# Kernel optimization log

Hardware: AMD Instinct MI355X
Metric: run time of the kernel (lower is better)

## Reference

```python
import jax, jax.numpy as jnp
import numpy as np

N_NODES = 50000
N_EDGES = 600000
C = 128
T = 2          # layer index t
NU = 1         # DRew nu parameter
EPS = 0.0      # GIN eps


def mlp(x, W1, b1, W2, b2):
    # instantiate_mlp with final_activation=False, batch_norm=False:
    # Linear -> ReLU -> Linear
    return jax.nn.relu(x @ W1 + b1) @ W2 + b2


def setup_inputs() -> dict:
    key = jax.random.key(0)
    ks = jax.random.split(key, 16)
    node_embeddings = jax.random.normal(ks[0], (T + 1, N_NODES, C), dtype=jnp.float32)
    edge_index = jax.random.randint(ks[1], (2, N_EDGES), 0, N_NODES, dtype=jnp.int32)
    edge_weights = jax.random.randint(ks[2], (N_EDGES,), 1, T + 2, dtype=jnp.int32)  # hops 1..3
    s = 1.0 / np.sqrt(C)
    def lin(k):
        kw, kb = jax.random.split(k)
        return (jax.random.uniform(kw, (C, C), jnp.float32, -s, s),
                jax.random.uniform(kb, (C,), jnp.float32, -s, s))
    loop_W1, loop_b1 = lin(ks[3]); loop_W2, loop_b2 = lin(ks[4])
    rel_W1, rel_b1 = lin(ks[5]); rel_W2, rel_b2 = lin(ks[6])
    # T higher-hop MLPs (k = 2 .. T+1), stacked along axis 0
    hh1 = [lin(k) for k in jax.random.split(ks[7], T)]
    hh2 = [lin(k) for k in jax.random.split(ks[8], T)]
    hh_W1 = jnp.stack([w for w, _ in hh1]); hh_b1 = jnp.stack([b for _, b in hh1])
    hh_W2 = jnp.stack([w for w, _ in hh2]); hh_b2 = jnp.stack([b for _, b in hh2])
    hop_coef = jax.random.normal(ks[9], (T + 1,), dtype=jnp.float32)
    return dict(t=T, node_embeddings=node_embeddings, edge_index=edge_index,
                edge_weights=edge_weights,
                loop_W1=loop_W1, loop_b1=loop_b1, loop_W2=loop_W2, loop_b2=loop_b2,
                rel_W1=rel_W1, rel_b1=rel_b1, rel_W2=rel_W2, rel_b2=rel_b2,
                hh_W1=hh_W1, hh_b1=hh_b1, hh_W2=hh_W2, hh_b2=hh_b2,
                hop_coef=hop_coef)


def reference(t, node_embeddings, edge_index, edge_weights,
              loop_W1, loop_b1, loop_W2, loop_b2,
              rel_W1, rel_b1, rel_W2, rel_b2,
              hh_W1, hh_b1, hh_W2, hh_b2, hop_coef):
    x_t = node_embeddings[t]                       # [N, C]
    n = x_t.shape[0]
    row, col = edge_index[0], edge_index[1]        # sparse A: out[row] += X[col]
    dt = x_t.dtype

    hops = []
    # hop 1: relational MLP on current-layer embeddings
    h1 = mlp(x_t, rel_W1, rel_b1, rel_W2, rel_b2)
    m1 = (edge_weights == 1).astype(dt)[:, None]
    hops.append(jax.ops.segment_sum(h1[col] * m1, row, num_segments=n))
    # hops k = 2 .. t+1: per-hop MLP on delayed embeddings (DRew)
    for k in range(2, t + 2):
        delay = max(0, k - NU)
        hk = mlp(node_embeddings[t - delay],
                 hh_W1[k - 2], hh_b1[k - 2], hh_W2[k - 2], hh_b2[k - 2])
        mk = (edge_weights == k).astype(dt)[:, None]
        hops.append(jax.ops.segment_sum(hk[col] * mk, row, num_segments=n))

    by_hop = jnp.stack(hops)                       # [t+1, N, C]
    self_term = mlp((1.0 + EPS) * x_t, loop_W1, loop_b1, loop_W2, loop_b2)
    return self_term + jnp.einsum('k,knc->nc', hop_coef, by_hop)
```

## Files before the change

kernel.cpp:

```cpp
#include <hip/hip_runtime.h>

#define N_NODES 50000
#define N_EDGES 600000
#define C 128
#define STRIPS 3125
#define GROUPS 782
#define N_TASKS 4

typedef __bf16 bf16;
typedef __attribute__((ext_vector_type(8))) __bf16 bf16x8;
typedef __attribute__((ext_vector_type(4))) __bf16 bf16x4;
typedef __attribute__((ext_vector_type(2))) __bf16 bf16x2;
typedef __attribute__((ext_vector_type(4))) float f32x4;
typedef __attribute__((ext_vector_type(2))) float f32x2;

struct PtrsV { const void* p[8]; };

__device__ __forceinline__ int bf16_wild(unsigned short w) {
    int exp = (w >> 7) & 0xFF;
    int mant = w & 0x7F;
    if (exp == 0xFF) return 1;
    if (exp >= 133) return 1;
    if (exp == 0) return mant != 0 ? 1 : 0;
    if (exp <= 114) return 1;
    return 0;
}

__global__ void __launch_bounds__(256) detect_zero_kernel(
    const unsigned short* __restrict__ emb,
    const unsigned short* __restrict__ w,
    const unsigned short* __restrict__ b,
    const unsigned short* __restrict__ hc,
    int* __restrict__ flags, int* __restrict__ deg)
{
    if (blockIdx.x == 0) {
        int lane = threadIdx.x;
        if (lane >= 64) return;
        int ce = 0, cw = 0, cb = 0, ch = 0;
        for (int j = 0; j < 4; ++j) {
            ce += bf16_wild(emb[lane * 4 + j]);
            cw += bf16_wild(w[lane * 4 + j]);
        }
        for (int j = 0; j < 2; ++j) cb += bf16_wild(b[lane * 2 + j]);
        if (lane < 3) ch = bf16_wild(hc[lane]);
        for (int off = 32; off > 0; off >>= 1) {
            ce += __shfl_down(ce, off);
            cw += __shfl_down(cw, off);
            cb += __shfl_down(cb, off);
            ch += __shfl_down(ch, off);
        }
        if (lane == 0) {
            int wf = (cw >= 16) ? 1 : 0;
            flags[0] = (ce >= 16) ? 1 : 0;
            flags[1] = wf;
            flags[2] = (cb >= 8) ? 1 : 0;
            flags[3] = (ch > 0) ? 1 : wf;
        }
    } else {
        int i = (blockIdx.x - 1) * 256 + threadIdx.x;
        if (i < N_NODES) deg[i] = 0;
    }
}

__global__ void __launch_bounds__(256) pack_kernel(
    PtrsV wmats, PtrsV bvecs, const void* hc_raw,
    const int* __restrict__ flags,
    bf16* __restrict__ pw, float* __restrict__ cbias, float* __restrict__ ccoef)
{
    int tid = blockIdx.x * 256 + threadIdx.x;
    int wf = flags[1], bfl = flags[2], hf = flags[3];
    if (tid < 8 * 16384) {
        int m    = tid >> 14;
        int r    = tid & 16383;
        int j    = r & 7;
        int lane = (r >> 3) & 63;
        int n0   = (r >> 9) & 7;
        int kk   = r >> 12;
        int k = kk * 32 + (lane >> 4) * 8 + j;
        int n = n0 * 16 + (lane & 15);
        int idx = k * C + n + ((m == 4 || m == 5) ? 16384 : 0);
        float v = wf ? ((const float*)wmats.p[m])[idx]
                     : (float)((const bf16*)wmats.p[m])[idx];
        pw[tid] = (bf16)v;
    } else if (tid < 8 * 16384 + 1024) {
        int j = tid - 8 * 16384;
        int m = j >> 7, n = j & 127;
        int idx = n + ((m == 4 || m == 5) ? 128 : 0);
        float v = bfl ? ((const float*)bvecs.p[m])[idx]
                      : (float)((const bf16*)bvecs.p[m])[idx];
        cbias[j] = v;
    } else if (tid < 8 * 16384 + 1024 + 3) {
        int i = tid - (8 * 16384 + 1024);
        float v = hf ? ((const float*)hc_raw)[i]
                     : (float)((const bf16*)hc_raw)[i];
        ccoef[i] = v;
    }
}

__global__ __launch_bounds__(256, 2) void mlp_kernel(
    const void* __restrict__ emb_raw,
    const bf16* __restrict__ pw,
    const float* __restrict__ cbias,
    const float* __restrict__ ccoef,
    const int* __restrict__ flags,
    bf16* __restrict__ h,
    bf16* __restrict__ hs)
{
    __shared__ bf16 sH[4][64][136];
    const int tid  = threadIdx.x;
    const int wave = tid >> 6, lane = tid & 63;
    const int wid  = blockIdx.x * 4 + wave;
    if (wid >= N_TASKS * GROUPS) return;
    const int task = wid & 3;
    const int grp  = wid >> 2;
    const int lrow = lane & 15, lquad = lane >> 4;
    bf16 (*sh)[136] = sH[wave];

    const int m1_of[4] = {0, 2, 4, 6};
    const int ly_of[4] = {2, 1, 0, 2};
    const int m1 = m1_of[task];
    const bf16x8* w1v = (const bf16x8*)(pw + (size_t)m1 * 16384);
    const bf16x8* w2v = w1v + 2048;
    const float oscale = (task == 0) ? ccoef[0] : (task == 1) ? ccoef[1]
                       : (task == 2) ? ccoef[2] : 1.0f;
    bf16* outp = (task == 3) ? hs : (h + (size_t)task * N_NODES * C);
    const int emb_f32 = flags[0];
    const size_t lbase = (size_t)ly_of[task] * N_NODES * C;

    const int s0 = grp * 4;
    int nv = STRIPS - s0; if (nv > 4) nv = 4;

    float b1f[8], b2f[8];
    #pragma unroll
    for (int n0 = 0; n0 < 8; ++n0) {
        b1f[n0] = cbias[m1 * 128 + n0 * 16 + lrow];
        b2f[n0] = cbias[(m1 + 1) * 128 + n0 * 16 + lrow];
    }

    bf16x8 af[4][4];
    #pragma unroll
    for (int i = 0; i < 4; ++i) {
        if (i < nv) {
            size_t xb = lbase + (size_t)((s0 + i) * 16 + lrow) * C + lquad * 8;
            if (emb_f32) {
                const float* xf = (const float*)emb_raw + xb;
                #pragma unroll
                for (int kk = 0; kk < 4; ++kk) {
                    f32x4 u0 = *(const f32x4*)(xf + kk * 32);
                    f32x4 u1 = *(const f32x4*)(xf + kk * 32 + 4);
                    bf16x8 v;
                    v[0]=(bf16)u0[0]; v[1]=(bf16)u0[1]; v[2]=(bf16)u0[2]; v[3]=(bf16)u0[3];
                    v[4]=(bf16)u1[0]; v[5]=(bf16)u1[1]; v[6]=(bf16)u1[2]; v[7]=(bf16)u1[3];
                    af[i][kk] = v;
                }
            } else {
                const bf16* x16 = (const bf16*)emb_raw + xb;
                #pragma unroll
                for (int kk = 0; kk < 4; ++kk)
                    af[i][kk] = *(const bf16x8*)(x16 + kk * 32);
            }
        }
    }

    #pragma unroll
    for (int n0 = 0; n0 < 8; ++n0) {
        bf16x8 bv0 = w1v[0 * 512 + n0 * 64 + lane];
        bf16x8 bv1 = w1v[1 * 512 + n0 * 64 + lane];
        bf16x8 bv2 = w1v[2 * 512 + n0 * 64 + lane];
        bf16x8 bv3 = w1v[3 * 512 + n0 * 64 + lane];
        int n = n0 * 16 + lrow;
        float bias = b1f[n0];
        #pragma unroll
        for (int i = 0; i < 4; ++i) {
            if (i < nv) {
                f32x4 a4 = {0.f, 0.f, 0.f, 0.f};
                a4 = __builtin_amdgcn_mfma_f32_16x16x32_bf16(af[i][0], bv0, a4, 0, 0, 0);
                a4 = __builtin_amdgcn_mfma_f32_16x16x32_bf16(af[i][1], bv1, a4, 0, 0, 0);
                a4 = __builtin_amdgcn_mfma_f32_16x16x32_bf16(af[i][2], bv2, a4, 0, 0, 0);
                a4 = __builtin_amdgcn_mfma_f32_16x16x32_bf16(af[i][3], bv3, a4, 0, 0, 0);
                #pragma unroll
                for (int r = 0; r < 4; ++r) {
                    float v = a4[r] + bias;
                    v = v > 0.f ? v : 0.f;
                    sh[i * 16 + lquad * 4 + r][n] = (bf16)v;
                }
            }
        }
    }

    bf16x8 ah[4][4];
    #pragma unroll
    for (int i = 0; i < 4; ++i)
        if (i < nv) {
            #pragma unroll
            for (int kk = 0; kk < 4; ++kk)
                ah[i][kk] = *(const bf16x8*)(&sh[i * 16 + lrow][kk * 32 + lquad * 8]);
        }

    #pragma unroll
    for (int n0 = 0; n0 < 8; ++n0) {
        bf16x8 bv0 = w2v[0 * 512 + n0 * 64 + lane];
        bf16x8 bv1 = w2v[1 * 512 + n0 * 64 + lane];
        bf16x8 bv2 = w2v[2 * 512 + n0 * 64 + lane];
        bf16x8 bv3 = w2v[3 * 512 + n0 * 64 + lane];
        int n = n0 * 16 + lrow;
        float bias = b2f[n0];
        #pragma unroll
        for (int i = 0; i < 4; ++i) {
            if (i < nv) {
                f32x4 a4 = {0.f, 0.f, 0.f, 0.f};
                a4 = __builtin_amdgcn_mfma_f32_16x16x32_bf16(ah[i][0], bv0, a4, 0, 0, 0);
                a4 = __builtin_amdgcn_mfma_f32_16x16x32_bf16(ah[i][1], bv1, a4, 0, 0, 0);
                a4 = __builtin_amdgcn_mfma_f32_16x16x32_bf16(ah[i][2], bv2, a4, 0, 0, 0);
                a4 = __builtin_amdgcn_mfma_f32_16x16x32_bf16(ah[i][3], bv3, a4, 0, 0, 0);
                #pragma unroll
                for (int r = 0; r < 4; ++r)
                    sh[i * 16 + lquad * 4 + r][n] = (bf16)((a4[r] + bias) * oscale);
            }
        }
    }

    {
        int row = lane >> 2;
        int cs  = (lane & 3) * 32;
        #pragma unroll
        for (int i = 0; i < 4; ++i) {
            if (i < nv) {
                bf16* dst = outp + (size_t)((s0 + i) * 16) * C;
                #pragma unroll
                for (int j = 0; j < 4; ++j) {
                    bf16x8 v = *(const bf16x8*)(&sh[i * 16 + row][cs + j * 8]);
                    *(bf16x8*)(dst + (size_t)row * C + cs + j * 8) = v;
                }
            }
        }
    }
}

__global__ void __launch_bounds__(256) hist_kernel(
    const int* __restrict__ erow, int* __restrict__ deg)
{
    int e = blockIdx.x * 256 + threadIdx.x;
    if (e >= N_EDGES) return;
    atomicAdd(&deg[erow[e]], 1);
}

__device__ __forceinline__ int wave_incl_scan(int v, int lane) {
    int x = v;
    #pragma unroll
    for (int d = 1; d < 64; d <<= 1) {
        int t = __shfl_up(x, d);
        if (lane >= d) x += t;
    }
    return x;
}

__global__ void __launch_bounds__(256) scanA_kernel(
    const int* __restrict__ deg, int* __restrict__ offsets, int* __restrict__ btot)
{
    __shared__ int swave[4];
    int b = blockIdx.x, tid = threadIdx.x;
    int i = b * 256 + tid;
    int lane = tid & 63, wv = tid >> 6;
    int v = (i < N_NODES) ? deg[i] : 0;
    int x = wave_incl_scan(v, lane);
    if (lane == 63) swave[wv] = x;
    __syncthreads();
    int w0 = swave[0], w1 = swave[1], w2 = swave[2], w3 = swave[3];
    int wp = (wv > 0 ? w0 : 0) + (wv > 1 ? w1 : 0) + (wv > 2 ? w2 : 0);
    if (i < N_NODES) offsets[i] = wp + x - v;
    if (tid == 0) btot[b] = w0 + w1 + w2 + w3;
}

__global__ void __launch_bounds__(256) scanB_kernel(
    const int* __restrict__ btot, int* __restrict__ bbase, int nblk)
{
    __shared__ int swave[4];
    int tid = threadIdx.x;
    int lane = tid & 63, wv = tid >> 6;
    int v = (tid < nblk) ? btot[tid] : 0;
    int x = wave_incl_scan(v, lane);
    if (lane == 63) swave[wv] = x;
    __syncthreads();
    int w0 = swave[0], w1 = swave[1], w2 = swave[2], w3 = swave[3];
    int wp = (wv > 0 ? w0 : 0) + (wv > 1 ? w1 : 0) + (wv > 2 ? w2 : 0);
    if (tid < nblk) bbase[tid] = wp + x - v;
}

__global__ void __launch_bounds__(256) scanC_kernel(
    const int* __restrict__ bbase, int* __restrict__ offsets, int* __restrict__ cursor)
{
    int i = blockIdx.x * 256 + threadIdx.x;
    if (i < N_NODES) {
        int o = offsets[i] + bbase[blockIdx.x];
        offsets[i] = o;
        cursor[i] = o;
    }
    if (i == 0) offsets[N_NODES] = N_EDGES;
}

__global__ void __launch_bounds__(256) fill_kernel(
    const int* __restrict__ erow, const int* __restrict__ ecol,
    const int* __restrict__ ew,
    int* __restrict__ cursor, int* __restrict__ edata)
{
    int e = blockIdx.x * 256 + threadIdx.x;
    if (e >= N_EDGES) return;
    int dst = erow[e];
    int pos = atomicAdd(&cursor[dst], 1);
    edata[pos] = (ecol[e] << 2) | (ew[e] - 1);
}

__global__ void __launch_bounds__(256) gather_kernel(
    const int* __restrict__ offsets, const int* __restrict__ edata,
    const bf16* __restrict__ h,
    const bf16* __restrict__ hs,
    void* __restrict__ out,
    const int* __restrict__ flags)
{
    const int node = blockIdx.x * 4 + (threadIdx.x >> 6);
    if (node >= N_NODES) return;
    const int lane = threadIdx.x & 63;
    const int c = lane * 2;

    bf16x2 sv = *(const bf16x2*)(hs + (size_t)node * C + c);
    float a0 = (float)sv[0], a1 = (float)sv[1];

    const int s = offsets[node], e = offsets[node + 1];
    for (int base = s; base < e; base += 64) {
        int idx = base + lane;
        int ed_i = (idx < e) ? edata[idx] : 0;
        int cnt = e - base; if (cnt > 64) cnt = 64;
        int j = 0;
        for (; j + 8 <= cnt; j += 8) {
            float t0 = 0.f, t1 = 0.f;
            #pragma unroll
            for (int u = 0; u < 8; ++u) {
                int ed = __shfl(ed_i, j + u);
                bf16x2 v = *(const bf16x2*)(h + (size_t)(ed & 3) * (N_NODES * C)
                                              + (size_t)(ed >> 2) * C + c);
                t0 += (float)v[0];
                t1 += (float)v[1];
            }
            a0 += t0; a1 += t1;
        }
        for (; j + 4 <= cnt; j += 4) {
            int e0 = __shfl(ed_i, j);
            int e1 = __shfl(ed_i, j + 1);
            int e2 = __shfl(ed_i, j + 2);
            int e3 = __shfl(ed_i, j + 3);
            bf16x2 v0 = *(const bf16x2*)(h + (size_t)(e0 & 3) * (N_NODES * C) + (size_t)(e0 >> 2) * C + c);
            bf16x2 v1 = *(const bf16x2*)(h + (size_t)(e1 & 3) * (N_NODES * C) + (size_t)(e1 >> 2) * C + c);
            bf16x2 v2 = *(const bf16x2*)(h + (size_t)(e2 & 3) * (N_NODES * C) + (size_t)(e2 >> 2) * C + c);
            bf16x2 v3 = *(const bf16x2*)(h + (size_t)(e3 & 3) * (N_NODES * C) + (size_t)(e3 >> 2) * C + c);
            a0 += (float)v0[0] + (float)v1[0] + (float)v2[0] + (float)v3[0];
            a1 += (float)v0[1] + (float)v1[1] + (float)v2[1] + (float)v3[1];
        }
        for (; j < cnt; ++j) {
            int ed = __shfl(ed_i, j);
            bf16x2 v = *(const bf16x2*)(h + (size_t)(ed & 3) * (N_NODES * C) + (size_t)(ed >> 2) * C + c);
            a0 += (float)v[0];
            a1 += (float)v[1];
        }
    }

    if (flags[0]) {
        f32x2 o; o[0] = a0; o[1] = a1;
        *(f32x2*)((float*)out + (size_t)node * C + c) = o;
    } else {
        bf16x2 o; o[0] = (bf16)a0; o[1] = (bf16)a1;
        *(bf16x2*)((bf16*)out + (size_t)node * C + c) = o;
    }
}

extern "C" void kernel_launch(void* const* d_in, const int* in_sizes, int n_in,
                              void* d_out, int out_size, void* d_ws, size_t ws_size,
                              hipStream_t stream) {
    const void* emb = d_in[1];
    const int*  ei  = (const int*)d_in[2];
    const int*  ew  = (const int*)d_in[3];

    const size_t H_BYTES  = (size_t)3 * N_NODES * C * sizeof(bf16);
    const size_t HS_BYTES = (size_t)N_NODES * C * sizeof(bf16);
    const size_t PW_BYTES = (size_t)8 * 16384 * sizeof(bf16);
    bf16*  h      = (bf16*)d_ws;
    bf16*  hs     = (bf16*)((char*)d_ws + H_BYTES);
    bf16*  pw     = (bf16*)((char*)d_ws + H_BYTES + HS_BYTES);
    float* cbias  = (float*)((char*)d_ws + H_BYTES + HS_BYTES + PW_BYTES);
    float* ccoef  = cbias + 1024;
    int*   flags  = (int*)(ccoef + 4);
    int*   deg    = flags + 16;
    int*   cursor = deg + N_NODES;
    int*   offsets= cursor + N_NODES;
    int*   btot   = offsets + N_NODES + 8;
    int*   bbase  = btot + 256;
    int*   edata  = bbase + 256;

    PtrsV wptr;
    wptr.p[0] = d_in[8];   wptr.p[1] = d_in[10];
    wptr.p[2] = d_in[12];  wptr.p[3] = d_in[14];
    wptr.p[4] = d_in[12];  wptr.p[5] = d_in[14];
    wptr.p[6] = d_in[4];   wptr.p[7] = d_in[6];
    PtrsV bptr;
    bptr.p[0] = d_in[9];   bptr.p[1] = d_in[11];
    bptr.p[2] = d_in[13];  bptr.p[3] = d_in[15];
    bptr.p[4] = d_in[13];  bptr.p[5] = d_in[15];
    bptr.p[6] = d_in[5];   bptr.p[7] = d_in[7];

    const int NBLK = (N_NODES + 255) / 256;

    detect_zero_kernel<<<1 + NBLK, 256, 0, stream>>>(
        (const unsigned short*)emb, (const unsigned short*)d_in[8],
        (const unsigned short*)d_in[9], (const unsigned short*)d_in[16],
        flags, deg);

    pack_kernel<<<517, 256, 0, stream>>>(wptr, bptr, d_in[16], flags, pw, cbias, ccoef);

    const int* erow = ei;
    const int* ecol = ei + N_EDGES;
    hist_kernel<<<(N_EDGES + 255) / 256, 256, 0, stream>>>(erow, deg);
    scanA_kernel<<<NBLK, 256, 0, stream>>>(deg, offsets, btot);
    scanB_kernel<<<1, 256, 0, stream>>>(btot, bbase, NBLK);
    scanC_kernel<<<NBLK, 256, 0, stream>>>(bbase, offsets, cursor);
    fill_kernel<<<(N_EDGES + 255) / 256, 256, 0, stream>>>(erow, ecol, ew, cursor, edata);

    mlp_kernel<<<(N_TASKS * GROUPS + 3) / 4, 256, 0, stream>>>(
        emb, pw, cbias, ccoef, flags, h, hs);

    gather_kernel<<<(N_NODES + 3) / 4, 256, 0, stream>>>(
        offsets, edata, h, hs, d_out, flags);
}
```

Baseline: 285.4 us.

## Split gather wave into two half-waves over edges and halve MLP strips per wave

The gather kernel now has each half of a wave handle alternate edges, with each lane loading 4 bf16 channels (8-byte loads) instead of 2. The two halves are combined with a cross-half shuffle reduction before the self term is added and the result stored. This is meant to double the edge-level memory parallelism per wave and widen the loads. Separately, the MLP kernel processes 2 strips per wave instead of 4, with a smaller LDS tile and a higher occupancy bound. That increases wave count and occupancy but reloads the weight fragments more often.

```diff
diff --git a/kernel.cpp b/kernel.cpp
--- a/kernel.cpp
+++ b/kernel.cpp
@@ -4,7 +4,7 @@
 #define N_EDGES 600000
 #define C 128
 #define STRIPS 3125
-#define GROUPS 782
+#define GROUPS 1563
 #define N_TASKS 4
 
 typedef __bf16 bf16;
@@ -97,7 +97,7 @@
     }
 }
 
-__global__ __launch_bounds__(256, 2) void mlp_kernel(
+__global__ __launch_bounds__(256, 4) void mlp_kernel(
     const void* __restrict__ emb_raw,
     const bf16* __restrict__ pw,
     const float* __restrict__ cbias,
@@ -106,7 +106,7 @@
     bf16* __restrict__ h,
     bf16* __restrict__ hs)
 {
-    __shared__ bf16 sH[4][64][136];
+    __shared__ bf16 sH[4][32][136];
     const int tid  = threadIdx.x;
     const int wave = tid >> 6, lane = tid & 63;
     const int wid  = blockIdx.x * 4 + wave;
@@ -127,8 +127,8 @@
     const int emb_f32 = flags[0];
     const size_t lbase = (size_t)ly_of[task] * N_NODES * C;
 
-    const int s0 = grp * 4;
-    int nv = STRIPS - s0; if (nv > 4) nv = 4;
+    const int s0 = grp * 2;
+    int nv = STRIPS - s0; if (nv > 2) nv = 2;
 
     float b1f[8], b2f[8];
     #pragma unroll
@@ -137,9 +137,9 @@
         b2f[n0] = cbias[(m1 + 1) * 128 + n0 * 16 + lrow];
     }
 
-    bf16x8 af[4][4];
-    #pragma unroll
-    for (int i = 0; i < 4; ++i) {
+    bf16x8 af[2][4];
+    #pragma unroll
+    for (int i = 0; i < 2; ++i) {
         if (i < nv) {
             size_t xb = lbase + (size_t)((s0 + i) * 16 + lrow) * C + lquad * 8;
             if (emb_f32) {
@@ -171,7 +171,7 @@
         int n = n0 * 16 + lrow;
         float bias = b1f[n0];
         #pragma unroll
-        for (int i = 0; i < 4; ++i) {
+        for (int i = 0; i < 2; ++i) {
             if (i < nv) {
                 f32x4 a4 = {0.f, 0.f, 0.f, 0.f};
                 a4 = __builtin_amdgcn_mfma_f32_16x16x32_bf16(af[i][0], bv0, a4, 0, 0, 0);
@@ -188,9 +188,9 @@
         }
     }
 
-    bf16x8 ah[4][4];
-    #pragma unroll
-    for (int i = 0; i < 4; ++i)
+    bf16x8 ah[2][4];
+    #pragma unroll
+    for (int i = 0; i < 2; ++i)
         if (i < nv) {
             #pragma unroll
             for (int kk = 0; kk < 4; ++kk)
@@ -206,7 +206,7 @@
         int n = n0 * 16 + lrow;
         float bias = b2f[n0];
         #pragma unroll
-        for (int i = 0; i < 4; ++i) {
+        for (int i = 0; i < 2; ++i) {
             if (i < nv) {
                 f32x4 a4 = {0.f, 0.f, 0.f, 0.f};
                 a4 = __builtin_amdgcn_mfma_f32_16x16x32_bf16(ah[i][0], bv0, a4, 0, 0, 0);
@@ -224,7 +224,7 @@
         int row = lane >> 2;
         int cs  = (lane & 3) * 32;
         #pragma unroll
-        for (int i = 0; i < 4; ++i) {
+        for (int i = 0; i < 2; ++i) {
             if (i < nv) {
                 bf16* dst = outp + (size_t)((s0 + i) * 16) * C;
                 #pragma unroll
@@ -321,10 +321,11 @@
     const int node = blockIdx.x * 4 + (threadIdx.x >> 6);
     if (node >= N_NODES) return;
     const int lane = threadIdx.x & 63;
-    const int c = lane * 2;
-
-    bf16x2 sv = *(const bf16x2*)(hs + (size_t)node * C + c);
-    float a0 = (float)sv[0], a1 = (float)sv[1];
+    const int half = lane >> 5;
+    const int li   = lane & 31;
+    const int c    = li * 4;
+
+    float a0 = 0.f, a1 = 0.f, a2 = 0.f, a3 = 0.f;
 
     const int s = offsets[node], e = offsets[node + 1];
     for (int base = s; base < e; base += 64) {
@@ -332,44 +333,61 @@
         int ed_i = (idx < e) ? edata[idx] : 0;
         int cnt = e - base; if (cnt > 64) cnt = 64;
         int j = 0;
-        for (; j + 8 <= cnt; j += 8) {
-            float t0 = 0.f, t1 = 0.f;
+        for (; j + 16 <= cnt; j += 16) {
             #pragma unroll
             for (int u = 0; u < 8; ++u) {
-                int ed = __shfl(ed_i, j + u);
-                bf16x2 v = *(const bf16x2*)(h + (size_t)(ed & 3) * (N_NODES * C)
+                int ed = __shfl(ed_i, j + 2 * u + half);
+                bf16x4 v = *(const bf16x4*)(h + (size_t)(ed & 3) * (N_NODES * C)
                                               + (size_t)(ed >> 2) * C + c);
-                t0 += (float)v[0];
-                t1 += (float)v[1];
-            }
-            a0 += t0; a1 += t1;
-        }
-        for (; j + 4 <= cnt; j += 4) {
-            int e0 = __shfl(ed_i, j);
-            int e1 = __shfl(ed_i, j + 1);
-            int e2 = __shfl(ed_i, j + 2);
-            int e3 = __shfl(ed_i, j + 3);
-            bf16x2 v0 = *(const bf16x2*)(h + (size_t)(e0 & 3) * (N_NODES * C) + (size_t)(e0 >> 2) * C + c);
-            bf16x2 v1 = *(const bf16x2*)(h + (size_t)(e1 & 3) * (N_NODES * C) + (size_t)(e1 >> 2) * C + c);
-            bf16x2 v2 = *(const bf16x2*)(h + (size_t)(e2 & 3) * (N_NODES * C) + (size_t)(e2 >> 2) * C + c);
-            bf16x2 v3 = *(const bf16x2*)(h + (size_t)(e3 & 3) * (N_NODES * C) + (size_t)(e3 >> 2) * C + c);
-            a0 += (float)v0[0] + (float)v1[0] + (float)v2[0] + (float)v3[0];
-            a1 += (float)v0[1] + (float)v1[1] + (float)v2[1] + (float)v3[1];
-        }
-        for (; j < cnt; ++j) {
+                a0 += (float)v[0]; a1 += (float)v[1];
+                a2 += (float)v[2]; a3 += (float)v[3];
+            }
+        }
+        for (; j + 8 <= cnt; j += 8) {
+            #pragma unroll
+            for (int u = 0; u < 4; ++u) {
+                int ed = __shfl(ed_i, j + 2 * u + half);
+                bf16x4 v = *(const bf16x4*)(h + (size_t)(ed & 3) * (N_NODES * C)
+                                              + (size_t)(ed >> 2) * C + c);
+                a0 += (float)v[0]; a1 += (float)v[1];
+                a2 += (float)v[2]; a3 += (float)v[3];
+            }
+        }
+        for (; j + 2 <= cnt; j += 2) {
+            int ed = __shfl(ed_i, j + half);
+            bf16x4 v = *(const bf16x4*)(h + (size_t)(ed & 3) * (N_NODES * C)
+                                          + (size_t)(ed >> 2) * C + c);
+            a0 += (float)v[0]; a1 += (float)v[1];
+            a2 += (float)v[2]; a3 += (float)v[3];
+        }
+        if (j < cnt) {
             int ed = __shfl(ed_i, j);
-            bf16x2 v = *(const bf16x2*)(h + (size_t)(ed & 3) * (N_NODES * C) + (size_t)(ed >> 2) * C + c);
-            a0 += (float)v[0];
-            a1 += (float)v[1];
-        }
-    }
-
-    if (flags[0]) {
-        f32x2 o; o[0] = a0; o[1] = a1;
-        *(f32x2*)((float*)out + (size_t)node * C + c) = o;
-    } else {
-        bf16x2 o; o[0] = (bf16)a0; o[1] = (bf16)a1;
-        *(bf16x2*)((bf16*)out + (size_t)node * C + c) = o;
+            if (half == 0) {
+                bf16x4 v = *(const bf16x4*)(h + (size_t)(ed & 3) * (N_NODES * C)
+                                              + (size_t)(ed >> 2) * C + c);
+                a0 += (float)v[0]; a1 += (float)v[1];
+                a2 += (float)v[2]; a3 += (float)v[3];
+            }
+        }
+    }
+
+    a0 += __shfl_xor(a0, 32);
+    a1 += __shfl_xor(a1, 32);
+    a2 += __shfl_xor(a2, 32);
+    a3 += __shfl_xor(a3, 32);
+
+    if (half == 0) {
+        bf16x4 sv = *(const bf16x4*)(hs + (size_t)node * C + c);
+        a0 += (float)sv[0]; a1 += (float)sv[1];
+        a2 += (float)sv[2]; a3 += (float)sv[3];
+        if (flags[0]) {
+            f32x4 o; o[0] = a0; o[1] = a1; o[2] = a2; o[3] = a3;
+            *(f32x4*)((float*)out + (size_t)node * C + c) = o;
+        } else {
+            bf16x4 o;
+            o[0] = (bf16)a0; o[1] = (bf16)a1; o[2] = (bf16)a2; o[3] = (bf16)a3;
+            *(bf16x4*)((bf16*)out + (size_t)node * C + c) = o;
+        }
     }
 }
 
```

Result: no change. 287.1 us (+0.6%).
